# Optimization experiments

Measured on AMD Instinct MI355X. Metric: run time of the kernel, lower is better.

## Reference

```python
import jax, jax.numpy as jnp
import numpy as np

N_NODES = 100000
N_EDGES = 1600000
N_GRAPHS = 128
BEHAVIOR_DIM = 32
LLM_DIM = 768
LLM_PROJ = 32
HIDDEN = 64
NUM_CLASSES = 2
INPUT_DIM = 64 + 16 + LLM_PROJ + BEHAVIOR_DIM  # 144


def gcn_conv(h, edge_index, edge_weight, W, b, n):
    """PyG GCNConv: linear -> gcn_norm with self-loops -> scatter-add at target."""
    h = h @ W  # [N, out]
    row, col = edge_index[0], edge_index[1]
    loop = jnp.arange(n)
    row_f = jnp.concatenate([row, loop])
    col_f = jnp.concatenate([col, loop])
    ew_f = jnp.concatenate([edge_weight, jnp.ones((n,), h.dtype)])
    deg = jax.ops.segment_sum(ew_f, col_f, num_segments=n)
    dinv = jnp.where(deg > 0, jax.lax.rsqrt(deg), 0.0)
    norm = dinv[row_f] * ew_f * dinv[col_f]  # [E+N]
    out = jax.ops.segment_sum(norm[:, None] * h[row_f], col_f, num_segments=n)
    return out + b


def global_mean_pool(x, batch, num_graphs):
    s = jax.ops.segment_sum(x, batch, num_segments=num_graphs)
    cnt = jax.ops.segment_sum(jnp.ones((x.shape[0],), x.dtype), batch, num_segments=num_graphs)
    return s / jnp.maximum(cnt, 1.0)[:, None]


def setup_inputs() -> dict:
    key = jax.random.key(0)
    ks = jax.random.split(key, 16)
    inp = {
        "x_names": jax.random.randint(ks[0], (N_NODES,), 0, 20000),
        "x_types": jax.random.randint(ks[1], (N_NODES,), 0, 100),
        "x_behaviors": jax.random.normal(ks[2], (N_NODES, BEHAVIOR_DIM), jnp.float32),
        "edge_index": jax.random.randint(ks[3], (2, N_EDGES), 0, N_NODES),
        "edge_weight": jax.random.uniform(ks[4], (N_EDGES,), jnp.float32),
        "batch": jnp.sort(jax.random.randint(ks[5], (N_NODES,), 0, N_GRAPHS)),
        "llm_features": jax.random.normal(ks[6], (N_NODES, LLM_DIM), jnp.float32),
        # parameters
        "name_emb": jax.random.normal(ks[7], (20000, 64), jnp.float32),
        "type_emb": jax.random.normal(ks[8], (100, 16), jnp.float32),
        "llm_proj_w": jax.random.normal(ks[9], (LLM_DIM, LLM_PROJ), jnp.float32) * 0.02,
        "llm_proj_b": jnp.zeros((LLM_PROJ,), jnp.float32),
        "conv1_w": jax.random.normal(ks[10], (INPUT_DIM, HIDDEN), jnp.float32) * 0.08,
        "conv1_b": jnp.zeros((HIDDEN,), jnp.float32),
        "conv2_w": jax.random.normal(ks[11], (HIDDEN, HIDDEN), jnp.float32) * 0.12,
        "conv2_b": jnp.zeros((HIDDEN,), jnp.float32),
        "cls_w": jax.random.normal(ks[12], (HIDDEN, NUM_CLASSES), jnp.float32) * 0.12,
        "cls_b": jnp.zeros((NUM_CLASSES,), jnp.float32),
    }
    return inp


def reference(x_names, x_types, x_behaviors, edge_index, edge_weight, batch,
              llm_features, name_emb, type_emb, llm_proj_w, llm_proj_b,
              conv1_w, conv1_b, conv2_w, conv2_b, cls_w, cls_b):
    n = x_names.shape[0]
    name_feat = name_emb[x_names]          # [N, 64]
    type_feat = type_emb[x_types]          # [N, 16]
    llm_feat = llm_features @ llm_proj_w + llm_proj_b  # [N, 32]
    x = jnp.concatenate([name_feat, type_feat, llm_feat, x_behaviors], axis=1)
    # dropout is identity in eval mode
    x = jax.nn.relu(gcn_conv(x, edge_index, edge_weight, conv1_w, conv1_b, n))
    x = jax.nn.relu(gcn_conv(x, edge_index, edge_weight, conv2_w, conv2_b, n))
    x = global_mean_pool(x, batch, N_GRAPHS)  # [G, HIDDEN]
    return x @ cls_w + cls_b                   # [G, 2]
```

## Files before the change

### kernel.cpp

```cpp
#include <hip/hip_runtime.h>
#include <cstdint>
#include <cstddef>

typedef __attribute__((ext_vector_type(8))) _Float16 f16x8;
typedef __attribute__((ext_vector_type(4))) _Float16 f16x4;
typedef __attribute__((ext_vector_type(4))) float f32x4;

__device__ __forceinline__ f16x8 cvt8(const float4& p, const float4& q) {
  f16x8 r;
  r[0] = (_Float16)p.x; r[1] = (_Float16)p.y; r[2] = (_Float16)p.z; r[3] = (_Float16)p.w;
  r[4] = (_Float16)q.x; r[5] = (_Float16)q.y; r[6] = (_Float16)q.z; r[7] = (_Float16)q.w;
  return r;
}

__device__ __forceinline__ void store4(_Float16* p, const float4& v) {
  f16x4 r;
  r[0] = (_Float16)v.x; r[1] = (_Float16)v.y; r[2] = (_Float16)v.z; r[3] = (_Float16)v.w;
  *(f16x4*)p = r;
}
__device__ __forceinline__ void store4(float* p, const float4& v) { *(float4*)p = v; }


__global__ void prep_kernel(const float* __restrict__ pw, const float* __restrict__ pb,
                            const float* __restrict__ w1, const float* __restrict__ w2,
                            _Float16* __restrict__ Bf, float* __restrict__ biasf,
                            _Float16* __restrict__ B2f, int* __restrict__ cnt, int n) {
  int idx = blockIdx.x * 256 + threadIdx.x;
  if (idx < n) cnt[idx] = 0;
  if (idx < 896 * 64) {
    int gk = idx >> 6, col = idx & 63;
    float val;
    if (gk < 768) {
      float acc = 0.0f;
      #pragma unroll 8
      for (int m = 0; m < 32; ++m) acc = fmaf(pw[gk * 32 + m], w1[(80 + m) * 64 + col], acc);
      val = acc;
    } else if (gk < 832) val = w1[(gk - 768) * 64 + col];
    else if (gk < 848)   val = w1[(64 + gk - 832) * 64 + col];
    else if (gk < 864)   val = w1[(112 + gk - 848) * 64 + col];
    else if (gk < 880)   val = w1[(128 + gk - 864) * 64 + col];
    else                 val = 0.0f;
    int chunk = gk >> 5, k = gk & 31;
    int g = k >> 3, j = k & 7;
    Bf[((size_t)(chunk * 4 + g) * 64 + col) * 8 + j] = (_Float16)val;
  } else if (idx < 896 * 64 + 64) {
    int col = idx - 896 * 64;
    float acc = 0.0f;
    for (int m = 0; m < 32; ++m) acc = fmaf(pb[m], w1[(80 + m) * 64 + col], acc);
    biasf[col] = acc;
  } else if (idx < 896 * 64 + 64 + 64 * 64) {
    int q2 = idx - (896 * 64 + 64);
    int gk = q2 >> 6, col = q2 & 63;
    float val = w2[gk * 64 + col];
    int chunk = gk >> 5, k = gk & 31;
    int g = k >> 3, j = k & 7;
    B2f[((size_t)(chunk * 4 + g) * 64 + col) * 8 + j] = (_Float16)val;
  }
}


__global__ void cnt_kernel(const int* __restrict__ ei, int* __restrict__ cnt, int E) {
  int e = blockIdx.x * 256 + threadIdx.x;
  if (e < E) atomicAdd(&cnt[ei[E + e]], 1);
}

__global__ __launch_bounds__(256) void scan_blk(const int* __restrict__ cnt,
                                                int* __restrict__ colp,
                                                int* __restrict__ bsum, int n) {
  __shared__ int ws[4];
  int t = threadIdx.x, lane = t & 63, w = t >> 6;
  int i = blockIdx.x * 256 + t;
  int v = (i < n) ? cnt[i] : 0;
  int x = v;
  #pragma unroll
  for (int off = 1; off < 64; off <<= 1) { int y = __shfl_up(x, off); if (lane >= off) x += y; }
  if (lane == 63) ws[w] = x;
  __syncthreads();
  if (t == 0) {
    int s = 0;
    #pragma unroll
    for (int k = 0; k < 4; ++k) { int tmp = ws[k]; ws[k] = s; s += tmp; }
    bsum[blockIdx.x] = s;
  }
  __syncthreads();
  if (i < n) colp[i] = ws[w] + x - v;
}

__global__ __launch_bounds__(512) void scan_top(int* __restrict__ bsum,
                                                int* __restrict__ colp, int nb, int n) {
  __shared__ int ws[8];
  int t = threadIdx.x, lane = t & 63, w = t >> 6;
  int v = (t < nb) ? bsum[t] : 0;
  int x = v;
  #pragma unroll
  for (int off = 1; off < 64; off <<= 1) { int y = __shfl_up(x, off); if (lane >= off) x += y; }
  if (lane == 63) ws[w] = x;
  __syncthreads();
  if (t == 0) {
    int s = 0;
    #pragma unroll
    for (int k = 0; k < 8; ++k) { int tmp = ws[k]; ws[k] = s; s += tmp; }
  }
  __syncthreads();
  int excl = ws[w] + x - v;
  if (t < nb) bsum[t] = excl;
  if (t == nb - 1) colp[n] = excl + v;
}

__global__ void scan_add(int* __restrict__ colp, const int* __restrict__ bsum, int n) {
  int i = blockIdx.x * 256 + threadIdx.x;
  if (i < n) colp[i] += bsum[blockIdx.x];
}

__global__ void fill_kernel(const int* __restrict__ ei, const float* __restrict__ ew,
                            int* __restrict__ colp, int2* __restrict__ csr, int E) {
  int e = blockIdx.x * 256 + threadIdx.x;
  if (e >= E) return;
  int row = ei[e], col = ei[E + e];
  int pos = atomicAdd(&colp[col], 1);
  csr[pos] = make_int2(row, __float_as_int(ew[e]));
}

__global__ void degsum_kernel(const int* __restrict__ colp, const int2* __restrict__ csr,
                              float* __restrict__ dinv, int n) {
  int j = blockIdx.x * 256 + threadIdx.x;
  if (j >= n) return;
  int e0 = (j > 0) ? colp[j - 1] : 0;
  int e1 = colp[j];
  float s = 1.0f;
  for (int e = e0; e < e1; ++e) s += __int_as_float(csr[e].y);
  dinv[j] = rsqrtf(s);
}


__device__ __forceinline__ void loadBf(const _Float16* __restrict__ Bf, int c, int g, int r16,
                                       f16x8 (&bf)[4]) {
  #pragma unroll
  for (int ct = 0; ct < 4; ++ct)
    bf[ct] = *(const f16x8*)(Bf + ((size_t)(c * 4 + g) * 64 + ct * 16 + r16) * 8);
}

__device__ __forceinline__ void mfma8(f32x4 (&acc)[2][4], const f16x8& a0, const f16x8& a1,
                                      const f16x8 (&bf)[4]) {
  #pragma unroll
  for (int ct = 0; ct < 4; ++ct) {
    acc[0][ct] = __builtin_amdgcn_mfma_f32_16x16x32_f16(a0, bf[ct], acc[0][ct], 0, 0, 0);
    acc[1][ct] = __builtin_amdgcn_mfma_f32_16x16x32_f16(a1, bf[ct], acc[1][ct], 0, 0, 0);
  }
}

__global__ __launch_bounds__(256, 3) void gemm1_kernel(
    const float* __restrict__ llm, const _Float16* __restrict__ Bf,
    const int* __restrict__ names, const int* __restrict__ types,
    const float* __restrict__ beh, const float* __restrict__ nemb,
    const float* __restrict__ temb, const float* __restrict__ biasf,
    const float* __restrict__ dinv, _Float16* __restrict__ out, int n)
{
  int nwg = gridDim.x;
  int b = blockIdx.x;
  int q = nwg >> 3, r = nwg & 7;
  int xcd = b & 7, bidx = b >> 3;
  int swz = (xcd < r ? xcd * (q + 1) : r * (q + 1) + (xcd - r) * q) + bidx;

  int w = swz * 4 + (threadIdx.x >> 6);
  int nw = (n + 31) >> 5;
  if (w >= nw) return;
  int lane = threadIdx.x & 63;
  int g = lane >> 4, r16 = lane & 15;
  int base = w * 32;

  int arow0 = base + r16;      if (arow0 > n - 1) arow0 = n - 1;
  int arow1 = base + 16 + r16; if (arow1 > n - 1) arow1 = n - 1;
  int nm0 = names[arow0], nm1 = names[arow1];
  int tp0 = types[arow0], tp1 = types[arow1];

  const float* pA0 = llm + (size_t)arow0 * 768 + g * 8;
  const float* pA1 = llm + (size_t)arow1 * 768 + g * 8;

  f32x4 acc[2][4];
  #pragma unroll
  for (int i = 0; i < 2; ++i)
    #pragma unroll
    for (int j = 0; j < 4; ++j) { acc[i][j][0] = 0.f; acc[i][j][1] = 0.f; acc[i][j][2] = 0.f; acc[i][j][3] = 0.f; }

  float4 X0l = *(const float4*)(pA0 +  0), X0h = *(const float4*)(pA0 +  4);
  float4 X1l = *(const float4*)(pA1 +  0), X1h = *(const float4*)(pA1 +  4);
  float4 Y0l = *(const float4*)(pA0 + 32), Y0h = *(const float4*)(pA0 + 36);
  float4 Y1l = *(const float4*)(pA1 + 32), Y1h = *(const float4*)(pA1 + 36);
  float4 Z0l = *(const float4*)(pA0 + 64), Z0h = *(const float4*)(pA0 + 68);
  float4 Z1l = *(const float4*)(pA1 + 64), Z1h = *(const float4*)(pA1 + 68);

  f16x8 bf[4], a0, a1;

  #pragma unroll 1
  for (int cc = 0; cc < 7; ++cc) {
    const int c = cc * 3;
    loadBf(Bf, c, g, r16, bf);
    a0 = cvt8(X0l, X0h); a1 = cvt8(X1l, X1h);
    X0l = *(const float4*)(pA0 + (c + 3) * 32);
    X0h = *(const float4*)(pA0 + (c + 3) * 32 + 4);
    X1l = *(const float4*)(pA1 + (c + 3) * 32);
    X1h = *(const float4*)(pA1 + (c + 3) * 32 + 4);
    __builtin_amdgcn_sched_barrier(0);
    mfma8(acc, a0, a1, bf);
    loadBf(Bf, c + 1, g, r16, bf);
    a0 = cvt8(Y0l, Y0h); a1 = cvt8(Y1l, Y1h);
    Y0l = *(const float4*)(pA0 + (c + 4) * 32);
    Y0h = *(const float4*)(pA0 + (c + 4) * 32 + 4);
    Y1l = *(const float4*)(pA1 + (c + 4) * 32);
    Y1h = *(const float4*)(pA1 + (c + 4) * 32 + 4);
    __builtin_amdgcn_sched_barrier(0);
    mfma8(acc, a0, a1, bf);
    loadBf(Bf, c + 2, g, r16, bf);
    a0 = cvt8(Z0l, Z0h); a1 = cvt8(Z1l, Z1h);
    Z0l = *(const float4*)(pA0 + (c + 5) * 32);
    Z0h = *(const float4*)(pA0 + (c + 5) * 32 + 4);
    Z1l = *(const float4*)(pA1 + (c + 5) * 32);
    Z1h = *(const float4*)(pA1 + (c + 5) * 32 + 4);
    __builtin_amdgcn_sched_barrier(0);
    mfma8(acc, a0, a1, bf);
  }

  loadBf(Bf, 21, g, r16, bf);
  a0 = cvt8(X0l, X0h); a1 = cvt8(X1l, X1h);
  mfma8(acc, a0, a1, bf);
  loadBf(Bf, 22, g, r16, bf);
  a0 = cvt8(Y0l, Y0h); a1 = cvt8(Y1l, Y1h);
  mfma8(acc, a0, a1, bf);
  loadBf(Bf, 23, g, r16, bf);
  a0 = cvt8(Z0l, Z0h); a1 = cvt8(Z1l, Z1h);
  mfma8(acc, a0, a1, bf);

  const float* pN0 = nemb + (size_t)nm0 * 64 + g * 8;
  const float* pN1 = nemb + (size_t)nm1 * 64 + g * 8;
  #pragma unroll
  for (int t = 0; t < 2; ++t) {
    float4 l0 = *(const float4*)(pN0 + t * 32), h0 = *(const float4*)(pN0 + t * 32 + 4);
    float4 l1 = *(const float4*)(pN1 + t * 32), h1 = *(const float4*)(pN1 + t * 32 + 4);
    loadBf(Bf, 24 + t, g, r16, bf);
    a0 = cvt8(l0, h0); a1 = cvt8(l1, h1);
    mfma8(acc, a0, a1, bf);
  }
  {
    const float* q0 = (g < 2) ? (temb + (size_t)tp0 * 16 + g * 8)
                              : (beh + (size_t)arow0 * 32 + (g - 2) * 8);
    const float* q1 = (g < 2) ? (temb + (size_t)tp1 * 16 + g * 8)
                              : (beh + (size_t)arow1 * 32 + (g - 2) * 8);
    float4 l0 = *(const float4*)q0, h0 = *(const float4*)(q0 + 4);
    float4 l1 = *(const float4*)q1, h1 = *(const float4*)(q1 + 4);
    loadBf(Bf, 26, g, r16, bf);
    a0 = cvt8(l0, h0); a1 = cvt8(l1, h1);
    mfma8(acc, a0, a1, bf);
  }
  {
    const float4 z = make_float4(0.f, 0.f, 0.f, 0.f);
    const float* r0 = beh + (size_t)arow0 * 32 + 16 + (g & 1) * 8;
    const float* r1 = beh + (size_t)arow1 * 32 + 16 + (g & 1) * 8;
    float4 l0 = *(const float4*)r0, h0 = *(const float4*)(r0 + 4);
    float4 l1 = *(const float4*)r1, h1 = *(const float4*)(r1 + 4);
    if (g >= 2) { l0 = z; h0 = z; l1 = z; h1 = z; }
    loadBf(Bf, 27, g, r16, bf);
    a0 = cvt8(l0, h0); a1 = cvt8(l1, h1);
    mfma8(acc, a0, a1, bf);
  }

  float dv0[4], dv1[4];
  #pragma unroll
  for (int rr = 0; rr < 4; ++rr) {
    int n0 = base + g * 4 + rr;      dv0[rr] = dinv[n0 < n ? n0 : n - 1];
    int n1 = base + 16 + g * 4 + rr; dv1[rr] = dinv[n1 < n ? n1 : n - 1];
  }
  #pragma unroll
  for (int ct = 0; ct < 4; ++ct) {
    int col = ct * 16 + r16;
    float bfc = biasf[col];
    #pragma unroll
    for (int rr = 0; rr < 4; ++rr) {
      int node0 = base + g * 4 + rr;
      if (node0 < n) out[(size_t)node0 * 64 + col] = (_Float16)((acc[0][ct][rr] + bfc) * dv0[rr]);
      int node1 = base + 16 + g * 4 + rr;
      if (node1 < n) out[(size_t)node1 * 64 + col] = (_Float16)((acc[1][ct][rr] + bfc) * dv1[rr]);
    }
  }
}


__global__ __launch_bounds__(256, 4) void gemm2_kernel(
    const _Float16* __restrict__ h, const _Float16* __restrict__ B2f,
    const float* __restrict__ dinv, _Float16* __restrict__ out, int n)
{
  int w = blockIdx.x * 4 + (threadIdx.x >> 6);
  int nw = (n + 31) >> 5;
  if (w >= nw) return;
  int lane = threadIdx.x & 63;
  int g = lane >> 4, r16 = lane & 15;
  int base = w * 32;
  int arow0 = base + r16;      if (arow0 > n - 1) arow0 = n - 1;
  int arow1 = base + 16 + r16; if (arow1 > n - 1) arow1 = n - 1;

  f32x4 acc[2][4];
  #pragma unroll
  for (int i = 0; i < 2; ++i)
    #pragma unroll
    for (int j = 0; j < 4; ++j) { acc[i][j][0] = 0.f; acc[i][j][1] = 0.f; acc[i][j][2] = 0.f; acc[i][j][3] = 0.f; }

  #pragma unroll
  for (int c = 0; c < 2; ++c) {
    f16x8 bf[4];
    loadBf(B2f, c, g, r16, bf);
    f16x8 a0 = *(const f16x8*)(h + (size_t)arow0 * 64 + c * 32 + g * 8);
    f16x8 a1 = *(const f16x8*)(h + (size_t)arow1 * 64 + c * 32 + g * 8);
    mfma8(acc, a0, a1, bf);
  }

  float dv0[4], dv1[4];
  #pragma unroll
  for (int rr = 0; rr < 4; ++rr) {
    int n0 = base + g * 4 + rr;      dv0[rr] = dinv[n0 < n ? n0 : n - 1];
    int n1 = base + 16 + g * 4 + rr; dv1[rr] = dinv[n1 < n ? n1 : n - 1];
  }
  #pragma unroll
  for (int ct = 0; ct < 4; ++ct) {
    int col = ct * 16 + r16;
    #pragma unroll
    for (int rr = 0; rr < 4; ++rr) {
      int node0 = base + g * 4 + rr;
      if (node0 < n) out[(size_t)node0 * 64 + col] = (_Float16)(acc[0][ct][rr] * dv0[rr]);
      int node1 = base + 16 + g * 4 + rr;
      if (node1 < n) out[(size_t)node1 * 64 + col] = (_Float16)(acc[1][ct][rr] * dv1[rr]);
    }
  }
}


template <typename OUT>
__global__ __launch_bounds__(256) void agg_kernel(
    const _Float16* __restrict__ hp, const int* __restrict__ colp,
    const int2* __restrict__ csr, const float* __restrict__ dinv,
    const float* __restrict__ bias, OUT* __restrict__ out, int n)
{
  int wid = threadIdx.x >> 6, lane = threadIdx.x & 63;
  int j = blockIdx.x * 4 + wid;
  if (j >= n) return;
  int gid = lane >> 4, sl = lane & 15;
  int e0 = (j > 0) ? colp[j - 1] : 0;
  int e1 = colp[j];

  float4 s0 = make_float4(0.f, 0.f, 0.f, 0.f);
  float4 s1 = make_float4(0.f, 0.f, 0.f, 0.f);
  int e = e0 + gid;
  for (; e + 12 < e1; e += 16) {
    int2 m0 = csr[e], m1 = csr[e + 4], m2 = csr[e + 8], m3 = csr[e + 12];
    f16x4 v0 = *(const f16x4*)(hp + (size_t)m0.x * 64 + sl * 4);
    f16x4 v1 = *(const f16x4*)(hp + (size_t)m1.x * 64 + sl * 4);
    f16x4 v2 = *(const f16x4*)(hp + (size_t)m2.x * 64 + sl * 4);
    f16x4 v3 = *(const f16x4*)(hp + (size_t)m3.x * 64 + sl * 4);
    float w0 = __int_as_float(m0.y), w1 = __int_as_float(m1.y);
    float w2 = __int_as_float(m2.y), w3 = __int_as_float(m3.y);
    s0.x = fmaf(w0, (float)v0[0], s0.x); s0.y = fmaf(w0, (float)v0[1], s0.y);
    s0.z = fmaf(w0, (float)v0[2], s0.z); s0.w = fmaf(w0, (float)v0[3], s0.w);
    s1.x = fmaf(w1, (float)v1[0], s1.x); s1.y = fmaf(w1, (float)v1[1], s1.y);
    s1.z = fmaf(w1, (float)v1[2], s1.z); s1.w = fmaf(w1, (float)v1[3], s1.w);
    s0.x = fmaf(w2, (float)v2[0], s0.x); s0.y = fmaf(w2, (float)v2[1], s0.y);
    s0.z = fmaf(w2, (float)v2[2], s0.z); s0.w = fmaf(w2, (float)v2[3], s0.w);
    s1.x = fmaf(w3, (float)v3[0], s1.x); s1.y = fmaf(w3, (float)v3[1], s1.y);
    s1.z = fmaf(w3, (float)v3[2], s1.z); s1.w = fmaf(w3, (float)v3[3], s1.w);
  }
  for (; e < e1; e += 4) {
    int2 m = csr[e];
    f16x4 v = *(const f16x4*)(hp + (size_t)m.x * 64 + sl * 4);
    float w0 = __int_as_float(m.y);
    s0.x = fmaf(w0, (float)v[0], s0.x); s0.y = fmaf(w0, (float)v[1], s0.y);
    s0.z = fmaf(w0, (float)v[2], s0.z); s0.w = fmaf(w0, (float)v[3], s0.w);
  }
  float4 t = make_float4(s0.x + s1.x, s0.y + s1.y, s0.z + s1.z, s0.w + s1.w);
  t.x += __shfl_xor(t.x, 16); t.y += __shfl_xor(t.y, 16);
  t.z += __shfl_xor(t.z, 16); t.w += __shfl_xor(t.w, 16);
  t.x += __shfl_xor(t.x, 32); t.y += __shfl_xor(t.y, 32);
  t.z += __shfl_xor(t.z, 32); t.w += __shfl_xor(t.w, 32);

  if (gid == 0) {
    float dj = dinv[j];
    f16x4 h4 = *(const f16x4*)(hp + (size_t)j * 64 + sl * 4);
    float4 bb = *(const float4*)(bias + sl * 4);
    float4 r;
    r.x = fmaxf(fmaf(dj, (float)h4[0] + t.x, bb.x), 0.f);
    r.y = fmaxf(fmaf(dj, (float)h4[1] + t.y, bb.y), 0.f);
    r.z = fmaxf(fmaf(dj, (float)h4[2] + t.z, bb.z), 0.f);
    r.w = fmaxf(fmaf(dj, (float)h4[3] + t.w, bb.w), 0.f);
    store4(out + (size_t)j * 64 + sl * 4, r);
  }
}


__global__ __launch_bounds__(256) void pool_kernel(const float* __restrict__ x,
                                                   const int* __restrict__ batch,
                                                   float* __restrict__ pooled, int n) {
  __shared__ float red[4][64];
  __shared__ int range_s[2];
  int gph = blockIdx.x;
  int tid = threadIdx.x, wid = tid >> 6, lane = tid & 63;
  if (tid < 2) {
    int target = gph + tid;
    int lo = 0, hi = n;
    while (lo < hi) { int m = (lo + hi) >> 1; if (batch[m] < target) lo = m + 1; else hi = m; }
    range_s[tid] = lo;
  }
  __syncthreads();
  int lo = range_s[0], hi = range_s[1];
  float acc = 0.0f;
  for (int i = lo + wid; i < hi; i += 4) acc += x[(size_t)i * 64 + lane];
  red[wid][lane] = acc;
  __syncthreads();
  if (tid < 64) {
    float sum = red[0][lane] + red[1][lane] + red[2][lane] + red[3][lane];
    float cntf = (float)(hi - lo);
    pooled[gph * 64 + lane] = sum / fmaxf(cntf, 1.0f);
  }
}

__global__ void cls_kernel(const float* __restrict__ pooled, const float* __restrict__ cw,
                           const float* __restrict__ cb, float* __restrict__ out) {
  int t = threadIdx.x;
  int gph = t >> 1, c = t & 1;
  float acc = cb[c];
  #pragma unroll 8
  for (int k = 0; k < 64; ++k) acc = fmaf(pooled[gph * 64 + k], cw[k * 2 + c], acc);
  out[gph * 2 + c] = acc;
}


extern "C" void kernel_launch(void* const* d_in, const int* in_sizes, int n_in,
                              void* d_out, int out_size, void* d_ws, size_t ws_size,
                              hipStream_t stream) {
  const int*   x_names  = (const int*)  d_in[0];
  const int*   x_types  = (const int*)  d_in[1];
  const float* behav    = (const float*)d_in[2];
  const int*   ei       = (const int*)  d_in[3];
  const float* ew       = (const float*)d_in[4];
  const int*   batch    = (const int*)  d_in[5];
  const float* llm      = (const float*)d_in[6];
  const float* name_emb = (const float*)d_in[7];
  const float* type_emb = (const float*)d_in[8];
  const float* pw       = (const float*)d_in[9];
  const float* pb       = (const float*)d_in[10];
  const float* w1       = (const float*)d_in[11];
  const float* b1       = (const float*)d_in[12];
  const float* w2       = (const float*)d_in[13];
  const float* b2       = (const float*)d_in[14];
  const float* cw       = (const float*)d_in[15];
  const float* cb       = (const float*)d_in[16];

  const int N = in_sizes[0];
  const int E = in_sizes[4];
  const int nb = (N + 255) / 256;
  const int eb = (E + 255) / 256;
  const int gblocks = ((N + 31) / 32 + 3) / 4;

  char* p = (char*)d_ws;
  auto alloc = [&](size_t bytes) -> void* {
    void* r = (void*)p; p += (bytes + 255) & ~(size_t)255; return r;
  };
  float*     dinv   = (float*)    alloc((size_t)N * 4);
  int*       cnt    = (int*)      alloc((size_t)N * 4);
  int*       colp   = (int*)      alloc((size_t)(N + 1) * 4);
  int2*      csr    = (int2*)     alloc((size_t)E * 8);
  int*       bsum   = (int*)      alloc((size_t)(nb + 1) * 4);
  _Float16*  Bf     = (_Float16*) alloc((size_t)896 * 64 * 2);
  _Float16*  B2f    = (_Float16*) alloc((size_t)64 * 64 * 2);
  float*     biasf  = (float*)    alloc((size_t)64 * 4);
  _Float16*  hp1    = (_Float16*) alloc((size_t)N * 64 * 2);
  _Float16*  y1     = (_Float16*) alloc((size_t)N * 64 * 2);
  _Float16*  hp2    = (_Float16*) alloc((size_t)N * 64 * 2);
  float*     y2     = (float*)    alloc((size_t)N * 64 * 4);
  float*     pooled = (float*)    alloc((size_t)128 * 64 * 4);
  (void)ws_size; (void)n_in; (void)out_size;

  int prep_blocks = (896 * 64 + 64 + 64 * 64 + 255) / 256;
  if (prep_blocks < nb) prep_blocks = nb;
  prep_kernel<<<prep_blocks, 256, 0, stream>>>(pw, pb, w1, w2, Bf, biasf, B2f, cnt, N);
  cnt_kernel<<<eb, 256, 0, stream>>>(ei, cnt, E);
  scan_blk<<<nb, 256, 0, stream>>>(cnt, colp, bsum, N);
  scan_top<<<1, 512, 0, stream>>>(bsum, colp, nb, N);
  scan_add<<<nb, 256, 0, stream>>>(colp, bsum, N);
  fill_kernel<<<eb, 256, 0, stream>>>(ei, ew, colp, csr, E);
  degsum_kernel<<<nb, 256, 0, stream>>>(colp, csr, dinv, N);

  gemm1_kernel<<<gblocks, 256, 0, stream>>>(llm, Bf, x_names, x_types, behav,
                                            name_emb, type_emb, biasf, dinv, hp1, N);
  agg_kernel<_Float16><<<(N + 3) / 4, 256, 0, stream>>>(hp1, colp, csr, dinv, b1, y1, N);
  gemm2_kernel<<<gblocks, 256, 0, stream>>>(y1, B2f, dinv, hp2, N);
  agg_kernel<float><<<(N + 3) / 4, 256, 0, stream>>>(hp2, colp, csr, dinv, b2, y2, N);
  pool_kernel<<<128, 256, 0, stream>>>(y2, batch, pooled, N);
  cls_kernel<<<1, 256, 0, stream>>>(pooled, cw, cb, (float*)d_out);
}
```

Measured before the change: 496.4 us.

## Fuse degree computation into count pass and restructure aggregation per-lane gathers

Weighted in-degrees are now accumulated with float atomics during the edge-count pass. The rsqrt is applied inside scan_add, which removes the separate degsum kernel and its second pass over the CSR. A separate fill pointer array keeps colp as start offsets, so aggregation reads colp[j] and colp[j+1]. The aggregation kernel is rewritten so each lane owns one feature column: edge metadata is loaded once per 64 edges and broadcast with shuffles, and eight gathers are kept in flight. The trade-offs are extra float atomic traffic, non-deterministic summation order, and narrower 2-byte per-lane gathers.

```diff
diff --git a/kernel.cpp b/kernel.cpp
--- a/kernel.cpp
+++ b/kernel.cpp
@@ -13,20 +13,14 @@
   return r;
 }
 
-__device__ __forceinline__ void store4(_Float16* p, const float4& v) {
-  f16x4 r;
-  r[0] = (_Float16)v.x; r[1] = (_Float16)v.y; r[2] = (_Float16)v.z; r[3] = (_Float16)v.w;
-  *(f16x4*)p = r;
-}
-__device__ __forceinline__ void store4(float* p, const float4& v) { *(float4*)p = v; }
-
 
 __global__ void prep_kernel(const float* __restrict__ pw, const float* __restrict__ pb,
                             const float* __restrict__ w1, const float* __restrict__ w2,
                             _Float16* __restrict__ Bf, float* __restrict__ biasf,
-                            _Float16* __restrict__ B2f, int* __restrict__ cnt, int n) {
+                            _Float16* __restrict__ B2f, int* __restrict__ cnt,
+                            float* __restrict__ deg, int n) {
   int idx = blockIdx.x * 256 + threadIdx.x;
-  if (idx < n) cnt[idx] = 0;
+  if (idx < n) { cnt[idx] = 0; deg[idx] = 1.0f; }
   if (idx < 896 * 64) {
     int gk = idx >> 6, col = idx & 63;
     float val;
@@ -37,8 +31,7 @@
       val = acc;
     } else if (gk < 832) val = w1[(gk - 768) * 64 + col];
     else if (gk < 848)   val = w1[(64 + gk - 832) * 64 + col];
-    else if (gk < 864)   val = w1[(112 + gk - 848) * 64 + col];
-    else if (gk < 880)   val = w1[(128 + gk - 864) * 64 + col];
+    else if (gk < 880)   val = w1[(112 + gk - 848) * 64 + col];
     else                 val = 0.0f;
     int chunk = gk >> 5, k = gk & 31;
     int g = k >> 3, j = k & 7;
@@ -59,9 +52,13 @@
 }
 
 
-__global__ void cnt_kernel(const int* __restrict__ ei, int* __restrict__ cnt, int E) {
+__global__ void cnt_kernel(const int* __restrict__ ei, const float* __restrict__ ew,
+                           int* __restrict__ cnt, float* __restrict__ deg, int E) {
   int e = blockIdx.x * 256 + threadIdx.x;
-  if (e < E) atomicAdd(&cnt[ei[E + e]], 1);
+  if (e >= E) return;
+  int col = ei[E + e];
+  atomicAdd(&cnt[col], 1);
+  atomicAdd(&deg[col], ew[e]);
 }
 
 __global__ __launch_bounds__(256) void scan_blk(const int* __restrict__ cnt,
@@ -107,29 +104,24 @@
   if (t == nb - 1) colp[n] = excl + v;
 }
 
-__global__ void scan_add(int* __restrict__ colp, const int* __restrict__ bsum, int n) {
+__global__ void scan_add(int* __restrict__ colp, int* __restrict__ fillp,
+                         const int* __restrict__ bsum, float* __restrict__ deg, int n) {
   int i = blockIdx.x * 256 + threadIdx.x;
-  if (i < n) colp[i] += bsum[blockIdx.x];
+  if (i < n) {
+    int c = colp[i] + bsum[blockIdx.x];
+    colp[i] = c;
+    fillp[i] = c;
+    deg[i] = rsqrtf(deg[i]);
+  }
 }
 
 __global__ void fill_kernel(const int* __restrict__ ei, const float* __restrict__ ew,
-                            int* __restrict__ colp, int2* __restrict__ csr, int E) {
+                            int* __restrict__ fillp, int2* __restrict__ csr, int E) {
   int e = blockIdx.x * 256 + threadIdx.x;
   if (e >= E) return;
   int row = ei[e], col = ei[E + e];
-  int pos = atomicAdd(&colp[col], 1);
+  int pos = atomicAdd(&fillp[col], 1);
   csr[pos] = make_int2(row, __float_as_int(ew[e]));
-}
-
-__global__ void degsum_kernel(const int* __restrict__ colp, const int2* __restrict__ csr,
-                              float* __restrict__ dinv, int n) {
-  int j = blockIdx.x * 256 + threadIdx.x;
-  if (j >= n) return;
-  int e0 = (j > 0) ? colp[j - 1] : 0;
-  int e1 = colp[j];
-  float s = 1.0f;
-  for (int e = e0; e < e1; ++e) s += __int_as_float(csr[e].y);
-  dinv[j] = rsqrtf(s);
 }
 
 
@@ -243,9 +235,9 @@
   }
   {
     const float* q0 = (g < 2) ? (temb + (size_t)tp0 * 16 + g * 8)
-                              : (beh + (size_t)arow0 * 32 + (g - 2) * 8);
+                              : (beh + (size_t)arow0 * 32 + (size_t)(g - 2) * 8);
     const float* q1 = (g < 2) ? (temb + (size_t)tp1 * 16 + g * 8)
-                              : (beh + (size_t)arow1 * 32 + (g - 2) * 8);
+                              : (beh + (size_t)arow1 * 32 + (size_t)(g - 2) * 8);
     float4 l0 = *(const float4*)q0, h0 = *(const float4*)(q0 + 4);
     float4 l1 = *(const float4*)q1, h1 = *(const float4*)(q1 + 4);
     loadBf(Bf, 26, g, r16, bf);
@@ -254,8 +246,8 @@
   }
   {
     const float4 z = make_float4(0.f, 0.f, 0.f, 0.f);
-    const float* r0 = beh + (size_t)arow0 * 32 + 16 + (g & 1) * 8;
-    const float* r1 = beh + (size_t)arow1 * 32 + 16 + (g & 1) * 8;
+    const float* r0 = beh + (size_t)arow0 * 32 + 16 + (size_t)(g & 1) * 8;
+    const float* r1 = beh + (size_t)arow1 * 32 + 16 + (size_t)(g & 1) * 8;
     float4 l0 = *(const float4*)r0, h0 = *(const float4*)(r0 + 4);
     float4 l1 = *(const float4*)r1, h1 = *(const float4*)(r1 + 4);
     if (g >= 2) { l0 = z; h0 = z; l1 = z; h1 = z; }
@@ -333,6 +325,9 @@
 }
 
 
+__device__ __forceinline__ void storeOut(_Float16* p, float v) { *p = (_Float16)v; }
+__device__ __forceinline__ void storeOut(float* p, float v) { *p = v; }
+
 template <typename OUT>
 __global__ __launch_bounds__(256) void agg_kernel(
     const _Float16* __restrict__ hp, const int* __restrict__ colp,
@@ -342,54 +337,45 @@
   int wid = threadIdx.x >> 6, lane = threadIdx.x & 63;
   int j = blockIdx.x * 4 + wid;
   if (j >= n) return;
-  int gid = lane >> 4, sl = lane & 15;
-  int e0 = (j > 0) ? colp[j - 1] : 0;
-  int e1 = colp[j];
-
-  float4 s0 = make_float4(0.f, 0.f, 0.f, 0.f);
-  float4 s1 = make_float4(0.f, 0.f, 0.f, 0.f);
-  int e = e0 + gid;
-  for (; e + 12 < e1; e += 16) {
-    int2 m0 = csr[e], m1 = csr[e + 4], m2 = csr[e + 8], m3 = csr[e + 12];
-    f16x4 v0 = *(const f16x4*)(hp + (size_t)m0.x * 64 + sl * 4);
-    f16x4 v1 = *(const f16x4*)(hp + (size_t)m1.x * 64 + sl * 4);
-    f16x4 v2 = *(const f16x4*)(hp + (size_t)m2.x * 64 + sl * 4);
-    f16x4 v3 = *(const f16x4*)(hp + (size_t)m3.x * 64 + sl * 4);
-    float w0 = __int_as_float(m0.y), w1 = __int_as_float(m1.y);
-    float w2 = __int_as_float(m2.y), w3 = __int_as_float(m3.y);
-    s0.x = fmaf(w0, (float)v0[0], s0.x); s0.y = fmaf(w0, (float)v0[1], s0.y);
-    s0.z = fmaf(w0, (float)v0[2], s0.z); s0.w = fmaf(w0, (float)v0[3], s0.w);
-    s1.x = fmaf(w1, (float)v1[0], s1.x); s1.y = fmaf(w1, (float)v1[1], s1.y);
-    s1.z = fmaf(w1, (float)v1[2], s1.z); s1.w = fmaf(w1, (float)v1[3], s1.w);
-    s0.x = fmaf(w2, (float)v2[0], s0.x); s0.y = fmaf(w2, (float)v2[1], s0.y);
-    s0.z = fmaf(w2, (float)v2[2], s0.z); s0.w = fmaf(w2, (float)v2[3], s0.w);
-    s1.x = fmaf(w3, (float)v3[0], s1.x); s1.y = fmaf(w3, (float)v3[1], s1.y);
-    s1.z = fmaf(w3, (float)v3[2], s1.z); s1.w = fmaf(w3, (float)v3[3], s1.w);
-  }
-  for (; e < e1; e += 4) {
-    int2 m = csr[e];
-    f16x4 v = *(const f16x4*)(hp + (size_t)m.x * 64 + sl * 4);
-    float w0 = __int_as_float(m.y);
-    s0.x = fmaf(w0, (float)v[0], s0.x); s0.y = fmaf(w0, (float)v[1], s0.y);
-    s0.z = fmaf(w0, (float)v[2], s0.z); s0.w = fmaf(w0, (float)v[3], s0.w);
-  }
-  float4 t = make_float4(s0.x + s1.x, s0.y + s1.y, s0.z + s1.z, s0.w + s1.w);
-  t.x += __shfl_xor(t.x, 16); t.y += __shfl_xor(t.y, 16);
-  t.z += __shfl_xor(t.z, 16); t.w += __shfl_xor(t.w, 16);
-  t.x += __shfl_xor(t.x, 32); t.y += __shfl_xor(t.y, 32);
-  t.z += __shfl_xor(t.z, 32); t.w += __shfl_xor(t.w, 32);
-
-  if (gid == 0) {
-    float dj = dinv[j];
-    f16x4 h4 = *(const f16x4*)(hp + (size_t)j * 64 + sl * 4);
-    float4 bb = *(const float4*)(bias + sl * 4);
-    float4 r;
-    r.x = fmaxf(fmaf(dj, (float)h4[0] + t.x, bb.x), 0.f);
-    r.y = fmaxf(fmaf(dj, (float)h4[1] + t.y, bb.y), 0.f);
-    r.z = fmaxf(fmaf(dj, (float)h4[2] + t.z, bb.z), 0.f);
-    r.w = fmaxf(fmaf(dj, (float)h4[3] + t.w, bb.w), 0.f);
-    store4(out + (size_t)j * 64 + sl * 4, r);
-  }
+  float dj = dinv[j];
+  float hj = (float)hp[(size_t)j * 64 + lane];
+  int e0 = colp[j], e1 = colp[j + 1];
+
+  float s0 = 0.0f, s1 = 0.0f;
+  for (int ebase = e0; ebase < e1; ebase += 64) {
+    int cnt = e1 - ebase; if (cnt > 64) cnt = 64;
+    int2 meta = (ebase + lane < e1) ? csr[ebase + lane] : make_int2(j, 0);
+    int cr = (cnt + 7) & ~7;
+    #pragma unroll 1
+    for (int i = 0; i < cr; i += 8) {
+      int sA = __shfl(meta.x, i + 0), sB = __shfl(meta.x, i + 1);
+      int sC = __shfl(meta.x, i + 2), sD = __shfl(meta.x, i + 3);
+      int sE = __shfl(meta.x, i + 4), sF = __shfl(meta.x, i + 5);
+      int sG = __shfl(meta.x, i + 6), sH = __shfl(meta.x, i + 7);
+      int wA = __shfl(meta.y, i + 0), wB = __shfl(meta.y, i + 1);
+      int wC = __shfl(meta.y, i + 2), wD = __shfl(meta.y, i + 3);
+      int wE = __shfl(meta.y, i + 4), wF = __shfl(meta.y, i + 5);
+      int wG = __shfl(meta.y, i + 6), wH = __shfl(meta.y, i + 7);
+      float fA = (float)hp[(size_t)sA * 64 + lane];
+      float fB = (float)hp[(size_t)sB * 64 + lane];
+      float fC = (float)hp[(size_t)sC * 64 + lane];
+      float fD = (float)hp[(size_t)sD * 64 + lane];
+      float fE = (float)hp[(size_t)sE * 64 + lane];
+      float fF = (float)hp[(size_t)sF * 64 + lane];
+      float fG = (float)hp[(size_t)sG * 64 + lane];
+      float fH = (float)hp[(size_t)sH * 64 + lane];
+      s0 = fmaf(__int_as_float(wA), fA, s0);
+      s1 = fmaf(__int_as_float(wB), fB, s1);
+      s0 = fmaf(__int_as_float(wC), fC, s0);
+      s1 = fmaf(__int_as_float(wD), fD, s1);
+      s0 = fmaf(__int_as_float(wE), fE, s0);
+      s1 = fmaf(__int_as_float(wF), fF, s1);
+      s0 = fmaf(__int_as_float(wG), fG, s0);
+      s1 = fmaf(__int_as_float(wH), fH, s1);
+    }
+  }
+  float acc = bias[lane] + dj * (hj + s0 + s1);
+  storeOut(out + (size_t)j * 64 + lane, fmaxf(acc, 0.0f));
 }
 
 
@@ -464,6 +450,7 @@
   float*     dinv   = (float*)    alloc((size_t)N * 4);
   int*       cnt    = (int*)      alloc((size_t)N * 4);
   int*       colp   = (int*)      alloc((size_t)(N + 1) * 4);
+  int*       fillp  = (int*)      alloc((size_t)N * 4);
   int2*      csr    = (int2*)     alloc((size_t)E * 8);
   int*       bsum   = (int*)      alloc((size_t)(nb + 1) * 4);
   _Float16*  Bf     = (_Float16*) alloc((size_t)896 * 64 * 2);
@@ -478,13 +465,12 @@
 
   int prep_blocks = (896 * 64 + 64 + 64 * 64 + 255) / 256;
   if (prep_blocks < nb) prep_blocks = nb;
-  prep_kernel<<<prep_blocks, 256, 0, stream>>>(pw, pb, w1, w2, Bf, biasf, B2f, cnt, N);
-  cnt_kernel<<<eb, 256, 0, stream>>>(ei, cnt, E);
+  prep_kernel<<<prep_blocks, 256, 0, stream>>>(pw, pb, w1, w2, Bf, biasf, B2f, cnt, dinv, N);
+  cnt_kernel<<<eb, 256, 0, stream>>>(ei, ew, cnt, dinv, E);
   scan_blk<<<nb, 256, 0, stream>>>(cnt, colp, bsum, N);
   scan_top<<<1, 512, 0, stream>>>(bsum, colp, nb, N);
-  scan_add<<<nb, 256, 0, stream>>>(colp, bsum, N);
-  fill_kernel<<<eb, 256, 0, stream>>>(ei, ew, colp, csr, E);
-  degsum_kernel<<<nb, 256, 0, stream>>>(colp, csr, dinv, N);
+  scan_add<<<nb, 256, 0, stream>>>(colp, fillp, bsum, dinv, N);
+  fill_kernel<<<eb, 256, 0, stream>>>(ei, ew, fillp, csr, E);
 
   gemm1_kernel<<<gblocks, 256, 0, stream>>>(llm, Bf, x_names, x_types, behav,
                                             name_emb, type_emb, biasf, dinv, hp1, N);
```

After: 534.5 us. 7.7% more time.
